# Optimization experiments

Measured on AMD Instinct MI355X. Metric: run time of the kernel, lower is better.

## Reference

```python
import jax, jax.numpy as jnp
import numpy as np

K = 3  # kernel_size
PAD = (K - 1) // 2


def _extract_patches(x):
    # x: (B, C, H, W) -> patches (B, C, K, K, H, W), matching F.unfold layout
    B, C, H, W = x.shape
    xp = jnp.pad(x, ((0, 0), (0, 0), (PAD, PAD), (PAD, PAD)))
    rows = []
    for dy in range(K):
        cols = [xp[:, :, dy:dy + H, dx:dx + W] for dx in range(K)]
        rows.append(jnp.stack(cols, axis=2))  # (B, C, K, H, W)
    return jnp.stack(rows, axis=2)  # (B, C, K, K, H, W)


def setup_inputs() -> dict:
    key = jax.random.key(0)
    k1, k2 = jax.random.split(key)
    B, Cin, Cout, Hs, Ws = 64, 64, 64, 64, 64
    x = jax.random.normal(k1, (B, Cin, Hs, Ws), dtype=jnp.float32)
    # weights: (h_size, w_size, out_channels, in_channels, K, K), scaled by 1/in_channels
    weights = jax.random.normal(k2, (Hs, Ws, Cout, Cin, K, K), dtype=jnp.float32) / Cin
    return {"x": x, "weights": weights}


def reference(x, weights):
    # Locally-connected conv: distinct (out,in,K,K) filter per spatial location.
    patches = _extract_patches(x)  # (B, in, K, K, h, w)
    # weights: i=h, j=w, a=out, b=in, c,d=K; patches: r=batch, b=in, c,d=K, i=h, j=w
    out = jnp.einsum('ijabcd,rbcdij->raij', weights, patches)  # (B, out, h, w)
    return jax.nn.relu(out)  # final_layer=False -> ReLU
```

## Files before the change

kernel.cpp:

```cpp
#include <hip/hip_runtime.h>

typedef short bf16x8 __attribute__((ext_vector_type(8)));
typedef float f32x4  __attribute__((ext_vector_type(4)));
typedef unsigned short u16x4 __attribute__((ext_vector_type(4)));

#define LSTR 296

__device__ __forceinline__ unsigned short f2bf(float f) {
    unsigned u = __float_as_uint(f);
    return (unsigned short)((u + 0x7FFFu + ((u >> 16) & 1u)) >> 16);
}

__global__ __launch_bounds__(256)
void transpose_in(const float* __restrict__ x, unsigned short* __restrict__ xT) {
    __shared__ float tile[64][65];
    const int t  = threadIdx.x;
    const int tr = blockIdx.x >> 6, tc = blockIdx.x & 63;
    const int r0 = tr << 6, c0 = tc << 6;
    const int cc = (t & 15) << 2;
    #pragma unroll
    for (int q = 0; q < 4; ++q) {
        const int rr = (t >> 4) + (q << 4);
        const f32x4 v = __builtin_nontemporal_load(
            (const f32x4*)&x[(size_t)(r0 + rr) * 4096 + c0 + cc]);
        tile[rr][cc + 0] = v[0]; tile[rr][cc + 1] = v[1];
        tile[rr][cc + 2] = v[2]; tile[rr][cc + 3] = v[3];
    }
    __syncthreads();
    #pragma unroll
    for (int q = 0; q < 4; ++q) {
        const int rr = (t >> 4) + (q << 4);
        u16x4 o;
        o[0] = f2bf(tile[cc + 0][rr]); o[1] = f2bf(tile[cc + 1][rr]);
        o[2] = f2bf(tile[cc + 2][rr]); o[3] = f2bf(tile[cc + 3][rr]);
        *(u16x4*)&xT[(size_t)(c0 + rr) * 4096 + r0 + cc] = o;
    }
}

__global__ __launch_bounds__(256)
void transpose_out_bf(const unsigned short* __restrict__ src, float* __restrict__ dst) {
    __shared__ unsigned short tile[64][66];
    const int t  = threadIdx.x;
    const int tr = blockIdx.x >> 6, tc = blockIdx.x & 63;
    const int r0 = tr << 6, c0 = tc << 6;
    const int cc = (t & 15) << 2;
    #pragma unroll
    for (int q = 0; q < 4; ++q) {
        const int rr = (t >> 4) + (q << 4);
        const u16x4 v = __builtin_nontemporal_load(
            (const u16x4*)&src[(size_t)(r0 + rr) * 4096 + c0 + cc]);
        tile[rr][cc + 0] = v[0]; tile[rr][cc + 1] = v[1];
        tile[rr][cc + 2] = v[2]; tile[rr][cc + 3] = v[3];
    }
    __syncthreads();
    #pragma unroll
    for (int q = 0; q < 4; ++q) {
        const int rr = (t >> 4) + (q << 4);
        f32x4 o;
        o[0] = __uint_as_float((unsigned)tile[cc + 0][rr] << 16);
        o[1] = __uint_as_float((unsigned)tile[cc + 1][rr] << 16);
        o[2] = __uint_as_float((unsigned)tile[cc + 2][rr] << 16);
        o[3] = __uint_as_float((unsigned)tile[cc + 3][rr] << 16);
        __builtin_nontemporal_store(o, (f32x4*)&dst[(size_t)(c0 + rr) * 4096 + r0 + cc]);
    }
}

__global__ __launch_bounds__(256, 4)
void lc_main(const unsigned short* __restrict__ xT, const float* __restrict__ wt,
             unsigned short* __restrict__ outT) {
    __shared__ __align__(16) unsigned short A[64 * LSTR];

    const int bid = blockIdx.x;
    const int swz = (bid & 7) * 512 + (bid >> 3);
    const int h   = swz >> 6;
    const int wq  = swz & 63;

    const int t    = threadIdx.x;
    const int lane = t & 63;
    const int wv   = t >> 6;

    const float* wloc = wt + (size_t)((h << 6) + wq) * 36864;
    const int co = (wv << 4) + (lane & 15);
    const int kg = lane >> 4;
    const float* wrow = wloc + co * 576 + (kg << 3);

    f32x4 acc[4] = {{0.f,0.f,0.f,0.f},{0.f,0.f,0.f,0.f},
                    {0.f,0.f,0.f,0.f},{0.f,0.f,0.f,0.f}};

    const int b_st = t >> 2;
    const int cig  = t & 3;

    f32x4 pb[3][2];
    pb[0][0] = __builtin_nontemporal_load((const f32x4*)(wrow + 0));
    pb[0][1] = __builtin_nontemporal_load((const f32x4*)(wrow + 4));
    pb[1][0] = __builtin_nontemporal_load((const f32x4*)(wrow + 32));
    pb[1][1] = __builtin_nontemporal_load((const f32x4*)(wrow + 36));

    bf16x8 xr[9];
    #pragma unroll
    for (int tap = 0; tap < 9; ++tap) {
        const int y  = h + tap / 3 - 1;
        const int xx = wq + tap % 3 - 1;
        bf16x8 v = {0,0,0,0,0,0,0,0};
        if ((unsigned)y < 64u && (unsigned)xx < 64u)
            v = *(const bf16x8*)&xT[(size_t)((y << 6) + xx) * 4096 + (b_st << 6) + (cig << 3)];
        xr[tap] = v;
    }
    {
        unsigned short* dst = &A[b_st * LSTR + cig * 72];
        #pragma unroll
        for (int tap = 0; tap < 9; ++tap)
            #pragma unroll
            for (int j = 0; j < 8; ++j)
                dst[j * 9 + tap] = (unsigned short)xr[tap][j];
    }
    #pragma unroll
    for (int tap = 0; tap < 9; ++tap) {
        const int y  = h + tap / 3 - 1;
        const int xx = wq + tap % 3 - 1;
        bf16x8 v = {0,0,0,0,0,0,0,0};
        if ((unsigned)y < 64u && (unsigned)xx < 64u)
            v = *(const bf16x8*)&xT[(size_t)((y << 6) + xx) * 4096 + (b_st << 6) + 32 + (cig << 3)];
        xr[tap] = v;
    }
    __syncthreads();

    #pragma unroll
    for (int ks = 0; ks < 18; ++ks) {
        if (ks == 9) {
            __syncthreads();
            unsigned short* dst = &A[b_st * LSTR + cig * 72];
            #pragma unroll
            for (int tap = 0; tap < 9; ++tap)
                #pragma unroll
                for (int j = 0; j < 8; ++j)
                    dst[j * 9 + tap] = (unsigned short)xr[tap][j];
            __syncthreads();
        }
        if (ks < 16) {
            const float* np = wrow + (ks + 2) * 32;
            pb[(ks + 2) % 3][0] = __builtin_nontemporal_load((const f32x4*)(np));
            pb[(ks + 2) % 3][1] = __builtin_nontemporal_load((const f32x4*)(np + 4));
        }
        const f32x4 lo = pb[ks % 3][0], hi = pb[ks % 3][1];
        bf16x8 bf;
        bf[0] = (short)f2bf(lo[0]); bf[1] = (short)f2bf(lo[1]);
        bf[2] = (short)f2bf(lo[2]); bf[3] = (short)f2bf(lo[3]);
        bf[4] = (short)f2bf(hi[0]); bf[5] = (short)f2bf(hi[1]);
        bf[6] = (short)f2bf(hi[2]); bf[7] = (short)f2bf(hi[3]);
        const int kk = (ks % 9) * 32 + (kg << 3);
        #pragma unroll
        for (int mt = 0; mt < 4; ++mt) {
            const bf16x8 af = *(const bf16x8*)&A[((mt << 4) + (lane & 15)) * LSTR + kk];
            acc[mt] = __builtin_amdgcn_mfma_f32_16x16x32_bf16(af, bf, acc[mt], 0, 0, 0);
        }
    }

    const int rg = lane >> 4;
    const size_t obase = (size_t)((h << 6) + wq) * 4096;
    #pragma unroll
    for (int mt = 0; mt < 4; ++mt) {
        #pragma unroll
        for (int j = 0; j < 4; ++j) {
            const int b = (mt << 4) + (rg << 2) + j;
            outT[obase + (b << 6) + co] = f2bf(fmaxf(acc[mt][j], 0.f));
        }
    }
}

__global__ __launch_bounds__(256, 4)
void lc_mfma(const float* __restrict__ x, const float* __restrict__ wt,
             float* __restrict__ out) {
    __shared__ __align__(16) unsigned short A[64 * LSTR];
    const int bid = blockIdx.x;
    const int swz = (bid & 7) * 512 + (bid >> 3);
    const int h   = swz >> 6;
    const int wq  = swz & 63;
    const int t    = threadIdx.x;
    const int lane = t & 63;
    const int wv   = t >> 6;
    const float* wloc = wt + (size_t)((h << 6) + wq) * 36864;
    const int co = (wv << 4) + (lane & 15);
    const int kg = lane >> 4;
    const float* wrow = wloc + co * 576 + (kg << 3);
    f32x4 acc[4] = {{0.f,0.f,0.f,0.f},{0.f,0.f,0.f,0.f},
                    {0.f,0.f,0.f,0.f},{0.f,0.f,0.f,0.f}};
    const int cil = t & 31;
    const int bro = t >> 5;
    for (int hs = 0; hs < 2; ++hs) {
        const int kbase = hs * 288;
        f32x4 pb[3][2];
        pb[0][0] = __builtin_nontemporal_load((const f32x4*)(wrow + kbase + 0));
        pb[0][1] = __builtin_nontemporal_load((const f32x4*)(wrow + kbase + 4));
        pb[1][0] = __builtin_nontemporal_load((const f32x4*)(wrow + kbase + 32));
        pb[1][1] = __builtin_nontemporal_load((const f32x4*)(wrow + kbase + 36));
        {
            const int ci = (hs << 5) + cil;
            for (int p = 0; p < 8; ++p) {
                const int b = (p << 3) + bro;
                const float* xb = x + ((size_t)((b << 6) + ci) << 12);
                unsigned short* dst = &A[b * LSTR + cil * 9];
                #pragma unroll
                for (int dy = 0; dy < 3; ++dy) {
                    const int y = h + dy - 1;
                    const bool yok = (unsigned)y < 64u;
                    #pragma unroll
                    for (int dx = 0; dx < 3; ++dx) {
                        const int xx = wq + dx - 1;
                        float v = 0.f;
                        if (yok && (unsigned)xx < 64u) v = xb[(y << 6) + xx];
                        dst[dy * 3 + dx] = f2bf(v);
                    }
                }
            }
        }
        __syncthreads();
        #pragma unroll
        for (int ks = 0; ks < 9; ++ks) {
            const int cur = ks % 3;
            const int nxt = (ks + 2) % 3;
            if (ks < 7) {
                const float* np = wrow + kbase + (ks + 2) * 32;
                pb[nxt][0] = __builtin_nontemporal_load((const f32x4*)(np));
                pb[nxt][1] = __builtin_nontemporal_load((const f32x4*)(np + 4));
            }
            const f32x4 lo = pb[cur][0], hi = pb[cur][1];
            bf16x8 bf;
            bf[0] = (short)f2bf(lo[0]); bf[1] = (short)f2bf(lo[1]);
            bf[2] = (short)f2bf(lo[2]); bf[3] = (short)f2bf(lo[3]);
            bf[4] = (short)f2bf(hi[0]); bf[5] = (short)f2bf(hi[1]);
            bf[6] = (short)f2bf(hi[2]); bf[7] = (short)f2bf(hi[3]);
            const int kk = (ks << 5) + (kg << 3);
            #pragma unroll
            for (int mt = 0; mt < 4; ++mt) {
                const bf16x8 af = *(const bf16x8*)&A[((mt << 4) + (lane & 15)) * LSTR + kk];
                acc[mt] = __builtin_amdgcn_mfma_f32_16x16x32_bf16(af, bf, acc[mt], 0, 0, 0);
            }
        }
        __syncthreads();
    }
    const int rg = lane >> 4;
    #pragma unroll
    for (int mt = 0; mt < 4; ++mt) {
        #pragma unroll
        for (int j = 0; j < 4; ++j) {
            const int b = (mt << 4) + (rg << 2) + j;
            out[(size_t)((b << 6) + co) * 4096 + (h << 6) + wq] = fmaxf(acc[mt][j], 0.f);
        }
    }
}

extern "C" void kernel_launch(void* const* d_in, const int* in_sizes, int n_in,
                              void* d_out, int out_size, void* d_ws, size_t ws_size,
                              hipStream_t stream) {
    const float* x  = (const float*)d_in[0];
    const float* wt = (const float*)d_in[1];
    float* out = (float*)d_out;

    const size_t xT_bytes   = (size_t)4096 * 4096 * 2;
    const size_t outT_bytes = (size_t)4096 * 4096 * 2;

    if (ws_size >= xT_bytes + outT_bytes) {
        unsigned short* xT   = (unsigned short*)d_ws;
        unsigned short* outT = (unsigned short*)((char*)d_ws + xT_bytes);
        hipLaunchKernelGGL(transpose_in, dim3(4096), dim3(256), 0, stream, x, xT);
        hipLaunchKernelGGL(lc_main, dim3(4096), dim3(256), 0, stream, xT, wt, outT);
        hipLaunchKernelGGL(transpose_out_bf, dim3(4096), dim3(256), 0, stream, outT, out);
    } else {
        hipLaunchKernelGGL(lc_mfma, dim3(4096), dim3(256), 0, stream, x, wt, out);
    }
}
```

Measured before the change: 200.2 us.

## Stage weights in LDS and load activations directly from global per wave

Restructures lc_main so the weights, not the activations, go through shared memory. Each block loads its fp32 weight chunk with coalesced loads, converts it to bf16 and scatters it into a double-buffered LDS tile in tap-major order, one chunk of 16 output channels at a time. Activation fragments for the MFMA are read straight from the transposed global input and prefetched in registers, and MFMAs for out-of-bounds taps are skipped. The aim is to coalesce the large weight stream and overlap its load with compute, at the cost of scattered 16-bit LDS stores and repeated global activation reads for each of the four chunks.

```diff
diff --git a/kernel.cpp b/kernel.cpp
--- a/kernel.cpp
+++ b/kernel.cpp
@@ -4,6 +4,8 @@
 typedef float f32x4  __attribute__((ext_vector_type(4)));
 typedef unsigned short u16x4 __attribute__((ext_vector_type(4)));
 
+#define BROW 584
+#define BBUF (16 * BROW)
 #define LSTR 296
 
 __device__ __forceinline__ unsigned short f2bf(float f) {
@@ -68,102 +70,105 @@
 __global__ __launch_bounds__(256, 4)
 void lc_main(const unsigned short* __restrict__ xT, const float* __restrict__ wt,
              unsigned short* __restrict__ outT) {
-    __shared__ __align__(16) unsigned short A[64 * LSTR];
+    __shared__ __align__(16) unsigned short Bs[2 * BBUF];
 
     const int bid = blockIdx.x;
     const int swz = (bid & 7) * 512 + (bid >> 3);
-    const int h   = swz >> 6;
-    const int wq  = swz & 63;
-
-    const int t    = threadIdx.x;
+    const int h = swz >> 6, wq = swz & 63;
+
+    const int t = threadIdx.x;
     const int lane = t & 63;
-    const int wv   = t >> 6;
-
-    const float* wloc = wt + (size_t)((h << 6) + wq) * 36864;
-    const int co = (wv << 4) + (lane & 15);
-    const int kg = lane >> 4;
-    const float* wrow = wloc + co * 576 + (kg << 3);
-
-    f32x4 acc[4] = {{0.f,0.f,0.f,0.f},{0.f,0.f,0.f,0.f},
-                    {0.f,0.f,0.f,0.f},{0.f,0.f,0.f,0.f}};
-
-    const int b_st = t >> 2;
-    const int cig  = t & 3;
-
-    f32x4 pb[3][2];
-    pb[0][0] = __builtin_nontemporal_load((const f32x4*)(wrow + 0));
-    pb[0][1] = __builtin_nontemporal_load((const f32x4*)(wrow + 4));
-    pb[1][0] = __builtin_nontemporal_load((const f32x4*)(wrow + 32));
-    pb[1][1] = __builtin_nontemporal_load((const f32x4*)(wrow + 36));
-
-    bf16x8 xr[9];
+    const int wv  = t >> 6;
+    const int l15 = lane & 15;
+    const int kg  = lane >> 4;
+
+    const float* wchunk0 = wt + (size_t)((h << 6) + wq) * 36864 + wv * 2304 + lane * 4;
+
+    int tapb[9]; int tval[9];
     #pragma unroll
     for (int tap = 0; tap < 9; ++tap) {
-        const int y  = h + tap / 3 - 1;
-        const int xx = wq + tap % 3 - 1;
-        bf16x8 v = {0,0,0,0,0,0,0,0};
-        if ((unsigned)y < 64u && (unsigned)xx < 64u)
-            v = *(const bf16x8*)&xT[(size_t)((y << 6) + xx) * 4096 + (b_st << 6) + (cig << 3)];
-        xr[tap] = v;
-    }
+        const int y = h + tap / 3 - 1, xx = wq + tap % 3 - 1;
+        const int ok = ((unsigned)y < 64u) && ((unsigned)xx < 64u);
+        tval[tap] = ok;
+        tapb[tap] = ok ? ((y << 6) + xx) : 0;
+    }
+
+    const unsigned short* aBase = xT + (((wv << 4) + l15) << 6) + (kg << 3);
+
+    unsigned short wa[36];
     {
-        unsigned short* dst = &A[b_st * LSTR + cig * 72];
-        #pragma unroll
-        for (int tap = 0; tap < 9; ++tap)
-            #pragma unroll
-            for (int j = 0; j < 8; ++j)
-                dst[j * 9 + tap] = (unsigned short)xr[tap][j];
-    }
-    #pragma unroll
-    for (int tap = 0; tap < 9; ++tap) {
-        const int y  = h + tap / 3 - 1;
-        const int xx = wq + tap % 3 - 1;
-        bf16x8 v = {0,0,0,0,0,0,0,0};
-        if ((unsigned)y < 64u && (unsigned)xx < 64u)
-            v = *(const bf16x8*)&xT[(size_t)((y << 6) + xx) * 4096 + (b_st << 6) + 32 + (cig << 3)];
-        xr[tap] = v;
-    }
-    __syncthreads();
-
-    #pragma unroll
-    for (int ks = 0; ks < 18; ++ks) {
-        if (ks == 9) {
-            __syncthreads();
-            unsigned short* dst = &A[b_st * LSTR + cig * 72];
-            #pragma unroll
-            for (int tap = 0; tap < 9; ++tap)
+        const int g0 = wv * 2304 + lane * 4;
+        #pragma unroll
+        for (int i = 0; i < 9; ++i) {
+            const int g = g0 + i * 256;
+            const int co = g / 576;
+            const int r = g - co * 576;
+            #pragma unroll
+            for (int j = 0; j < 4; ++j) {
+                const int ci = (r + j) / 9;
+                const int tap = (r + j) - ci * 9;
+                wa[i * 4 + j] = (unsigned short)(co * BROW + tap * 64 + ci);
+            }
+        }
+    }
+
+    f32x4 sreg[9];
+    const size_t obase = (size_t)((h << 6) + wq) * 4096;
+
+    {
+        const float* src = wchunk0;
+        #pragma unroll
+        for (int i = 0; i < 9; ++i)
+            sreg[i] = __builtin_nontemporal_load((const f32x4*)(src + i * 256));
+        #pragma unroll
+        for (int i = 0; i < 9; ++i)
+            #pragma unroll
+            for (int j = 0; j < 4; ++j)
+                Bs[wa[i * 4 + j]] = f2bf(sreg[i][j]);
+    }
+
+    #pragma unroll
+    for (int q = 0; q < 4; ++q) {
+        __syncthreads();
+        const unsigned short* Bq = &Bs[(q & 1) * BBUF];
+
+        bf16x8 af[4];
+        #pragma unroll
+        for (int p = 0; p < 4; ++p)
+            af[p] = *(const bf16x8*)(aBase + (size_t)tapb[p >> 1] * 4096 + ((p & 1) << 5));
+
+        if (q < 3) {
+            const float* src = wchunk0 + (q + 1) * 9216;
+            #pragma unroll
+            for (int i = 0; i < 9; ++i)
+                sreg[i] = __builtin_nontemporal_load((const f32x4*)(src + i * 256));
+        }
+
+        f32x4 acc = {0.f, 0.f, 0.f, 0.f};
+        #pragma unroll
+        for (int ks = 0; ks < 18; ++ks) {
+            const bf16x8 bf = *(const bf16x8*)&Bq[l15 * BROW + ks * 32 + (kg << 3)];
+            if (tval[ks >> 1])
+                acc = __builtin_amdgcn_mfma_f32_16x16x32_bf16(af[ks & 3], bf, acc, 0, 0, 0);
+            if (ks < 14)
+                af[ks & 3] = *(const bf16x8*)(aBase
+                    + (size_t)tapb[(ks + 4) >> 1] * 4096 + (((ks + 4) & 1) << 5));
+        }
+
+        #pragma unroll
+        for (int j = 0; j < 4; ++j) {
+            const int b = (wv << 4) + (kg << 2) + j;
+            const unsigned short v = f2bf(fmaxf(acc[j], 0.f));
+            __builtin_nontemporal_store(v, &outT[obase + (b << 6) + (q << 4) + l15]);
+        }
+
+        if (q < 3) {
+            unsigned short* dstb = &Bs[((q + 1) & 1) * BBUF];
+            #pragma unroll
+            for (int i = 0; i < 9; ++i)
                 #pragma unroll
-                for (int j = 0; j < 8; ++j)
-                    dst[j * 9 + tap] = (unsigned short)xr[tap][j];
-            __syncthreads();
-        }
-        if (ks < 16) {
-            const float* np = wrow + (ks + 2) * 32;
-            pb[(ks + 2) % 3][0] = __builtin_nontemporal_load((const f32x4*)(np));
-            pb[(ks + 2) % 3][1] = __builtin_nontemporal_load((const f32x4*)(np + 4));
-        }
-        const f32x4 lo = pb[ks % 3][0], hi = pb[ks % 3][1];
-        bf16x8 bf;
-        bf[0] = (short)f2bf(lo[0]); bf[1] = (short)f2bf(lo[1]);
-        bf[2] = (short)f2bf(lo[2]); bf[3] = (short)f2bf(lo[3]);
-        bf[4] = (short)f2bf(hi[0]); bf[5] = (short)f2bf(hi[1]);
-        bf[6] = (short)f2bf(hi[2]); bf[7] = (short)f2bf(hi[3]);
-        const int kk = (ks % 9) * 32 + (kg << 3);
-        #pragma unroll
-        for (int mt = 0; mt < 4; ++mt) {
-            const bf16x8 af = *(const bf16x8*)&A[((mt << 4) + (lane & 15)) * LSTR + kk];
-            acc[mt] = __builtin_amdgcn_mfma_f32_16x16x32_bf16(af, bf, acc[mt], 0, 0, 0);
-        }
-    }
-
-    const int rg = lane >> 4;
-    const size_t obase = (size_t)((h << 6) + wq) * 4096;
-    #pragma unroll
-    for (int mt = 0; mt < 4; ++mt) {
-        #pragma unroll
-        for (int j = 0; j < 4; ++j) {
-            const int b = (mt << 4) + (rg << 2) + j;
-            outT[obase + (b << 6) + co] = f2bf(fmaxf(acc[mt][j], 0.f));
+                for (int j = 0; j < 4; ++j)
+                    dstb[wa[i * 4 + j]] = f2bf(sreg[i][j]);
         }
     }
 }
@@ -233,8 +238,8 @@
             const int kk = (ks << 5) + (kg << 3);
             #pragma unroll
             for (int mt = 0; mt < 4; ++mt) {
-                const bf16x8 af = *(const bf16x8*)&A[((mt << 4) + (lane & 15)) * LSTR + kk];
-                acc[mt] = __builtin_amdgcn_mfma_f32_16x16x32_bf16(af, bf, acc[mt], 0, 0, 0);
+                const bf16x8 afl = *(const bf16x8*)&A[((mt << 4) + (lane & 15)) * LSTR + kk];
+                acc[mt] = __builtin_amdgcn_mfma_f32_16x16x32_bf16(afl, bf, acc[mt], 0, 0, 0);
             }
         }
         __syncthreads();
```

Result: slower. 251.7 us (+25.7%).
